# Kernel tuning notes

Hardware: AMD Instinct MI355X
Metric: run time of the kernel (lower is better)

The kernel has to match this reference:

```python
import jax, jax.numpy as jnp
import numpy as np

NUM_HEADS = 8
KEY_DIM = 64
WINDOW = 8
SHIFT = 4
B, H, W, C = 8, 64, 64, 512


def setup_inputs() -> dict:
    key = jax.random.key(0)
    ks = jax.random.split(key, 6)
    s = 0.02  # small init scale for numerically tame attention
    return {
        "x": jax.random.normal(ks[0], (B, H, W, C), jnp.float32),
        "wq": jax.random.normal(ks[1], (C, NUM_HEADS, KEY_DIM), jnp.float32) * s,
        "bq": jnp.zeros((NUM_HEADS, KEY_DIM), jnp.float32),
        "wk": jax.random.normal(ks[2], (C, NUM_HEADS, KEY_DIM), jnp.float32) * s,
        "bk": jnp.zeros((NUM_HEADS, KEY_DIM), jnp.float32),
        "wv": jax.random.normal(ks[3], (C, NUM_HEADS, KEY_DIM), jnp.float32) * s,
        "bv": jnp.zeros((NUM_HEADS, KEY_DIM), jnp.float32),
        "wo": jax.random.normal(ks[4], (NUM_HEADS, KEY_DIM, C), jnp.float32) * s,
        "bo": jnp.zeros((C,), jnp.float32),
    }


def reference(x, wq, bq, wk, bk, wv, bv, wo, bo):
    b, h, w, c = x.shape
    ws, ss = WINDOW, SHIFT
    pad_h = (ws - h % ws) % ws
    pad_w = (ws - w % ws) % ws
    padded = jnp.pad(x, ((0, 0), (0, pad_h), (0, pad_w), (0, 0)))
    if ss:
        padded = jnp.roll(padded, shift=(-ss, -ss), axis=(1, 2))
    ph, pw = h + pad_h, w + pad_w
    nh, nw = ph // ws, pw // ws
    # window partition: [B, nh, ws, nw, ws, C] -> [B*nh*nw, ws*ws, C]
    win = padded.reshape(b, nh, ws, nw, ws, c)
    win = win.transpose(0, 1, 3, 2, 4, 5).reshape(-1, ws * ws, c)
    q = jnp.einsum("ntc,chd->nthd", win, wq) + bq
    k = jnp.einsum("ntc,chd->nthd", win, wk) + bk
    v = jnp.einsum("ntc,chd->nthd", win, wv) + bv
    scale = 1.0 / jnp.sqrt(jnp.asarray(KEY_DIM, q.dtype))
    scores = jnp.einsum("nqhd,nkhd->nhqk", q, k) * scale
    attn = jax.nn.softmax(scores, axis=-1)
    out = jnp.einsum("nhqk,nkhd->nqhd", attn, v)
    proj = jnp.einsum("nqhd,hdc->nqc", out, wo) + bo
    # window merge
    merged = proj.reshape(b, nh, nw, ws, ws, c)
    merged = merged.transpose(0, 1, 3, 2, 4, 5).reshape(b, ph, pw, c)
    if ss:
        merged = jnp.roll(merged, shift=(ss, ss), axis=(1, 2))
    if pad_h or pad_w:
        merged = merged[:, :h, :w, :]
    return x + merged
```

## Files before the change

### kernel.cpp

```cpp
#include <hip/hip_runtime.h>

typedef unsigned short u16;
typedef short bf16x8 __attribute__((ext_vector_type(8)));
typedef float f32x4 __attribute__((ext_vector_type(4)));

typedef __attribute__((address_space(3))) unsigned int lds_uint;
typedef __attribute__((address_space(1))) const unsigned int glob_uint;

__device__ __forceinline__ void gll16(const void* g, void* l) {
    __builtin_amdgcn_global_load_lds((glob_uint*)g, (lds_uint*)l, 16, 0, 0);
}

__device__ __forceinline__ u16 f2b(float f) {
    union { float f; unsigned int u; } cv; cv.f = f;
    unsigned int u = cv.u;
    u += 0x7fffu + ((u >> 16) & 1u);
    return (u16)(u >> 16);
}

__device__ __forceinline__ uint2 pack4(float a, float b, float c, float d) {
    uint2 r;
    r.x = (unsigned int)f2b(a) | ((unsigned int)f2b(b) << 16);
    r.y = (unsigned int)f2b(c) | ((unsigned int)f2b(d) << 16);
    return r;
}

__global__ void prep_kernel(const float* __restrict__ wq, const float* __restrict__ wk,
                            const float* __restrict__ wv, const float* __restrict__ wo,
                            const float* __restrict__ bq, const float* __restrict__ bk,
                            const float* __restrict__ bv,
                            u16* __restrict__ wqkvh, u16* __restrict__ woT,
                            float* __restrict__ biash) {
    int idx = blockIdx.x * 256 + threadIdx.x;
    const int N1 = 512 * 1536;
    const int N2 = 512 * 512;
    if (idx < N1) {
        int k = idx / 1536, n2 = idx % 1536;
        int h = n2 / 192, j = n2 % 192;
        const float* w = (j < 64) ? wq : (j < 128) ? wk : wv;
        wqkvh[(size_t)n2 * 512 + k] = f2b(w[k * 512 + h * 64 + (j & 63)]);
    } else if (idx < N1 + N2) {
        int i = idx - N1;
        int k = i / 512, n = i % 512;
        woT[n * 512 + k] = f2b(wo[k * 512 + n]);
    } else if (idx < N1 + N2 + 1536) {
        int n2 = idx - N1 - N2;
        int h = n2 / 192, j = n2 % 192;
        const float* b = (j < 64) ? bq : (j < 128) ? bk : bv;
        biash[n2] = b[h * 64 + (j & 63)];
    }
}

__global__ __launch_bounds__(256) void pre_kernel(const float* __restrict__ x,
                                                  u16* __restrict__ xw) {
    int idx = blockIdx.x * 256 + threadIdx.x;
    int row = idx >> 6;
    int c = (idx & 63) * 8;
    int b_ = row >> 12, win = (row >> 6) & 63, t = row & 63;
    int wi = win >> 3, wj = win & 7, ti = t >> 3, tj = t & 7;
    int hh = (wi * 8 + ti + 4) & 63, ww = (wj * 8 + tj + 4) & 63;
    const float* src = x + ((size_t)b_ * 4096 + hh * 64 + ww) * 512 + c;
    float4 v0 = *(const float4*)src;
    float4 v1 = *(const float4*)(src + 4);
    ushort4 p0, p1;
    p0.x = f2b(v0.x); p0.y = f2b(v0.y); p0.z = f2b(v0.z); p0.w = f2b(v0.w);
    p1.x = f2b(v1.x); p1.y = f2b(v1.y); p1.z = f2b(v1.z); p1.w = f2b(v1.w);
    u16* dst = xw + (size_t)row * 512 + c;
    *(ushort4*)dst = p0;
    *(ushort4*)(dst + 4) = p1;
}

__global__ __launch_bounds__(256, 4) void fused_qkv_attn(const u16* __restrict__ xw,
        const u16* __restrict__ wqkvh, const float* __restrict__ biash,
        u16* __restrict__ ows) {
    __shared__ u16 S[16384];
    const int tid = threadIdx.x;
    const int lane = tid & 63, wid = tid >> 6;
    const int wr = wid >> 1, wc = wid & 1;
    const int m = lane & 15, qd = lane >> 4;
    const int win = blockIdx.x & 511;
    const int h = blockIdx.x >> 9;
    const int rowBase = win * 64;

    u16* As  = S;
    u16* Bs  = S + 4096;
    u16* QKs = S;
    u16* VT  = S + 8704;
    u16* Pw  = S + wid * 1152;

    const u16* Bsrc = wqkvh + (size_t)h * 192 * 512;
    f32x4 acc[2][6];
#pragma unroll
    for (int i = 0; i < 2; ++i)
#pragma unroll
        for (int j = 0; j < 6; ++j) acc[i][j] = (f32x4){0.f, 0.f, 0.f, 0.f};

    for (int kt = 0; kt < 8; ++kt) {
        const int k0 = kt * 64;
#pragma unroll
        for (int j = 0; j < 2; ++j) {
            int q = j * 256 + tid;
            int r = q >> 3, c = (q & 7) ^ (r & 7);
            gll16(xw + (size_t)(rowBase + r) * 512 + k0 + c * 8, As + q * 8);
        }
#pragma unroll
        for (int j = 0; j < 6; ++j) {
            int q = j * 256 + tid;
            int r = q >> 3, c = (q & 7) ^ (r & 7);
            gll16(Bsrc + (size_t)r * 512 + k0 + c * 8, Bs + q * 8);
        }
        __syncthreads();
#pragma unroll
        for (int s = 0; s < 2; ++s) {
            bf16x8 a[2], b[6];
#pragma unroll
            for (int ni = 0; ni < 6; ++ni) {
                int R = wc * 96 + ni * 16 + m;
                b[ni] = *(const bf16x8*)&Bs[R * 64 + (((s * 4 + qd) ^ (R & 7)) * 8)];
            }
#pragma unroll
            for (int mi = 0; mi < 2; ++mi) {
                int R = wr * 32 + mi * 16 + m;
                a[mi] = *(const bf16x8*)&As[R * 64 + (((s * 4 + qd) ^ (R & 7)) * 8)];
            }
#pragma unroll
            for (int mi = 0; mi < 2; ++mi)
#pragma unroll
                for (int ni = 0; ni < 6; ++ni)
                    acc[mi][ni] = __builtin_amdgcn_mfma_f32_16x16x32_bf16(b[ni], a[mi], acc[mi][ni], 0, 0, 0);
        }
        __syncthreads();
    }

#pragma unroll
    for (int mi = 0; mi < 2; ++mi) {
        int t = wr * 32 + mi * 16 + m;
#pragma unroll
        for (int ni = 0; ni < 6; ++ni) {
            int cn = wc * 96 + ni * 16;
            float4 bb = *(const float4*)&biash[h * 192 + cn + qd * 4];
            if (cn < 128) {
                *(uint2*)&QKs[t * 136 + cn + qd * 4] =
                    pack4(acc[mi][ni][0] + bb.x, acc[mi][ni][1] + bb.y,
                          acc[mi][ni][2] + bb.z, acc[mi][ni][3] + bb.w);
            } else {
                int d0 = cn - 128 + qd * 4;
                VT[(d0 + 0) * 72 + t] = f2b(acc[mi][ni][0] + bb.x);
                VT[(d0 + 1) * 72 + t] = f2b(acc[mi][ni][1] + bb.y);
                VT[(d0 + 2) * 72 + t] = f2b(acc[mi][ni][2] + bb.z);
                VT[(d0 + 3) * 72 + t] = f2b(acc[mi][ni][3] + bb.w);
            }
        }
    }
    __syncthreads();

    const int q0 = wid * 16;
    f32x4 sa[4];
#pragma unroll
    for (int ni = 0; ni < 4; ++ni) sa[ni] = (f32x4){0.f, 0.f, 0.f, 0.f};
#pragma unroll
    for (int s = 0; s < 2; ++s) {
        bf16x8 qf = *(const bf16x8*)&QKs[(q0 + m) * 136 + s * 32 + qd * 8];
#pragma unroll
        for (int ni = 0; ni < 4; ++ni) {
            bf16x8 kf = *(const bf16x8*)&QKs[(ni * 16 + m) * 136 + 64 + s * 32 + qd * 8];
            sa[ni] = __builtin_amdgcn_mfma_f32_16x16x32_bf16(qf, kf, sa[ni], 0, 0, 0);
        }
    }
    __syncthreads();

    const float c1 = 0.125f * 1.4426950408889634f;
#pragma unroll
    for (int rr = 0; rr < 4; ++rr) {
        float mx = -3.4e38f;
#pragma unroll
        for (int ni = 0; ni < 4; ++ni) mx = fmaxf(mx, sa[ni][rr]);
        mx = fmaxf(mx, __shfl_xor(mx, 1, 64));
        mx = fmaxf(mx, __shfl_xor(mx, 2, 64));
        mx = fmaxf(mx, __shfl_xor(mx, 4, 64));
        mx = fmaxf(mx, __shfl_xor(mx, 8, 64));
        float sum = 0.f;
#pragma unroll
        for (int ni = 0; ni < 4; ++ni) {
            float p = exp2f((sa[ni][rr] - mx) * c1);
            sa[ni][rr] = p;
            sum += p;
        }
        sum += __shfl_xor(sum, 1, 64);
        sum += __shfl_xor(sum, 2, 64);
        sum += __shfl_xor(sum, 4, 64);
        sum += __shfl_xor(sum, 8, 64);
        float inv = 1.f / sum;
        int r = qd * 4 + rr;
#pragma unroll
        for (int ni = 0; ni < 4; ++ni)
            Pw[r * 72 + ni * 16 + m] = f2b(sa[ni][rr] * inv);
    }

    f32x4 oa[4];
#pragma unroll
    for (int ni = 0; ni < 4; ++ni) oa[ni] = (f32x4){0.f, 0.f, 0.f, 0.f};
#pragma unroll
    for (int s = 0; s < 2; ++s) {
        bf16x8 pf = *(const bf16x8*)&Pw[m * 72 + s * 32 + qd * 8];
#pragma unroll
        for (int ni = 0; ni < 4; ++ni) {
            bf16x8 vf = *(const bf16x8*)&VT[(ni * 16 + m) * 72 + s * 32 + qd * 8];
            oa[ni] = __builtin_amdgcn_mfma_f32_16x16x32_bf16(vf, pf, oa[ni], 0, 0, 0);
        }
    }
    u16* dst = ows + (size_t)(rowBase + q0 + m) * 512 + h * 64;
#pragma unroll
    for (int ni = 0; ni < 4; ++ni)
        *(uint2*)&dst[ni * 16 + qd * 4] =
            pack4(oa[ni][0], oa[ni][1], oa[ni][2], oa[ni][3]);
}

__global__ __launch_bounds__(256) void proj_gemm(const u16* __restrict__ ows,
        const u16* __restrict__ woT, const float* __restrict__ bo,
        const float* __restrict__ x, float* __restrict__ out) {
    __shared__ u16 S[16384];
    u16* As = S;
    u16* Bs = S + 8192;
    const int tid = threadIdx.x;
    const int lane = tid & 63, wid = tid >> 6;
    const int wr = wid >> 1, wc = wid & 1;
    const int m = lane & 15, qd = lane >> 4;
    const int rowBase = blockIdx.y * 128;
    const int colBase = blockIdx.x * 128;
    const int c8 = (lane & 7) ^ (lane >> 3);

    f32x4 acc[4][4];
#pragma unroll
    for (int i = 0; i < 4; ++i)
#pragma unroll
        for (int j = 0; j < 4; ++j) acc[i][j] = (f32x4){0.f, 0.f, 0.f, 0.f};

    for (int kt = 0; kt < 8; ++kt) {
        const int k0 = kt * 64;
        __syncthreads();
#pragma unroll
        for (int j = 0; j < 4; ++j) {
            int q = (j * 4 + wid) * 64 + lane;
            int r = (j * 4 + wid) * 8 + (lane >> 3);
            gll16(ows + (size_t)(rowBase + r) * 512 + k0 + c8 * 8, &As[q * 8]);
            gll16(woT + (size_t)(colBase + r) * 512 + k0 + c8 * 8, &Bs[q * 8]);
        }
        __syncthreads();
#pragma unroll
        for (int s = 0; s < 2; ++s) {
            bf16x8 a[4], b[4];
#pragma unroll
            for (int ni = 0; ni < 4; ++ni) {
                int R = wc * 64 + ni * 16 + m;
                b[ni] = *(const bf16x8*)&Bs[R * 64 + (((s * 4 + qd) ^ (R & 7)) * 8)];
            }
#pragma unroll
            for (int mi = 0; mi < 4; ++mi) {
                int R = wr * 64 + mi * 16 + m;
                a[mi] = *(const bf16x8*)&As[R * 64 + (((s * 4 + qd) ^ (R & 7)) * 8)];
            }
#pragma unroll
            for (int mi = 0; mi < 4; ++mi)
#pragma unroll
                for (int ni = 0; ni < 4; ++ni)
                    acc[mi][ni] = __builtin_amdgcn_mfma_f32_16x16x32_bf16(b[ni], a[mi], acc[mi][ni], 0, 0, 0);
        }
    }
    __syncthreads();

    float* Ct = (float*)S;
    for (int p = 0; p < 2; ++p) {
        if (wr == p) {
#pragma unroll
            for (int mi = 0; mi < 4; ++mi) {
                int r = mi * 16 + m;
#pragma unroll
                for (int ni = 0; ni < 4; ++ni) {
                    int ch = (wc * 16 + ni * 4 + qd) ^ (r & 7);
                    *(f32x4*)&Ct[r * 128 + ch * 4] = acc[mi][ni];
                }
            }
        }
        __syncthreads();
        {
            int k = tid >> 2, cseg = tid & 3;
            int row = rowBase + p * 64 + k;
            int win = row >> 6, t = row & 63;
            int b_ = win >> 6, wh = (win >> 3) & 7, ww_ = win & 7;
            int ti = t >> 3, tj = t & 7;
            int hh = (wh * 8 + ti + 4) & 63;
            int www = (ww_ * 8 + tj + 4) & 63;
            size_t tok = (size_t)b_ * 4096 + hh * 64 + www;
            const float* xs = &x[tok * 512 + colBase + cseg * 32];
            const float* bs = &bo[colBase + cseg * 32];
            float* os = &out[tok * 512 + colBase + cseg * 32];
#pragma unroll
            for (int j = 0; j < 8; ++j) {
                int ch = (cseg * 8 + j) ^ (k & 7);
                f32x4 c = *(const f32x4*)&Ct[k * 128 + ch * 4];
                float4 xv = *(const float4*)&xs[j * 4];
                float4 bv = *(const float4*)&bs[j * 4];
                float4 o;
                o.x = c[0] + bv.x + xv.x;
                o.y = c[1] + bv.y + xv.y;
                o.z = c[2] + bv.z + xv.z;
                o.w = c[3] + bv.w + xv.w;
                *(float4*)&os[j * 4] = o;
            }
        }
        __syncthreads();
    }
}

extern "C" void kernel_launch(void* const* d_in, const int* in_sizes, int n_in,
                              void* d_out, int out_size, void* d_ws, size_t ws_size,
                              hipStream_t stream) {
    const float* x  = (const float*)d_in[0];
    const float* wq = (const float*)d_in[1];
    const float* bq = (const float*)d_in[2];
    const float* wk = (const float*)d_in[3];
    const float* bk = (const float*)d_in[4];
    const float* wv = (const float*)d_in[5];
    const float* bv = (const float*)d_in[6];
    const float* wo = (const float*)d_in[7];
    const float* bo = (const float*)d_in[8];
    float* out = (float*)d_out;
    char* ws = (char*)d_ws;

    u16*   wqkvh = (u16*)ws;
    u16*   woT   = (u16*)(ws + 1572864);
    float* biash = (float*)(ws + 1572864 + 524288);
    size_t off = 2103296;
    u16* xw  = (u16*)(ws + off);
    u16* ows = xw + (size_t)16777216;

    const int prepN = 512 * 1536 + 512 * 512 + 1536;
    prep_kernel<<<dim3((prepN + 255) / 256), dim3(256), 0, stream>>>(
        wq, wk, wv, wo, bq, bk, bv, wqkvh, woT, biash);
    pre_kernel<<<dim3(8192), dim3(256), 0, stream>>>(x, xw);
    fused_qkv_attn<<<dim3(4096), dim3(256), 0, stream>>>(xw, wqkvh, biash, ows);
    proj_gemm<<<dim3(4, 256), dim3(256), 0, stream>>>(ows, woT, bo, x, out);
}
```

Before: 257.9 us.

## Double-buffer QKV projection K-loop with 32-wide tiles and async prefetch

The QKV GEMM main loop now uses two LDS buffers with 32-wide K tiles. The next tile is prefetched via global_load_lds while the current one is computed, with explicit vmcnt waits and barriers in place of two __syncthreads per iteration. The LDS swizzle changes to match the narrower rows. The aim is to hide global load latency behind MFMA work, at the cost of more loop iterations, more barriers per K, and reliance on hand-tuned waitcnt counts.

```diff
diff --git a/kernel.cpp b/kernel.cpp
--- a/kernel.cpp
+++ b/kernel.cpp
@@ -82,55 +82,84 @@
     const int h = blockIdx.x >> 9;
     const int rowBase = win * 64;
 
-    u16* As  = S;
-    u16* Bs  = S + 4096;
+    u16* const A0 = S;
+    u16* const B0 = S + 2048;
+    u16* const A1 = S + 8192;
+    u16* const B1 = S + 10240;
     u16* QKs = S;
     u16* VT  = S + 8704;
     u16* Pw  = S + wid * 1152;
 
-    const u16* Bsrc = wqkvh + (size_t)h * 192 * 512;
+    const u16* xwRow = xw + (size_t)rowBase * 512;
+    const u16* Bsrc  = wqkvh + (size_t)h * 192 * 512;
+
+    const int rA = tid >> 2;
+    const int cA = (tid & 3) ^ ((rA >> 1) & 3);
+
     f32x4 acc[2][6];
 #pragma unroll
     for (int i = 0; i < 2; ++i)
 #pragma unroll
         for (int j = 0; j < 6; ++j) acc[i][j] = (f32x4){0.f, 0.f, 0.f, 0.f};
 
-    for (int kt = 0; kt < 8; ++kt) {
-        const int k0 = kt * 64;
-#pragma unroll
-        for (int j = 0; j < 2; ++j) {
-            int q = j * 256 + tid;
-            int r = q >> 3, c = (q & 7) ^ (r & 7);
-            gll16(xw + (size_t)(rowBase + r) * 512 + k0 + c * 8, As + q * 8);
-        }
-#pragma unroll
-        for (int j = 0; j < 6; ++j) {
-            int q = j * 256 + tid;
-            int r = q >> 3, c = (q & 7) ^ (r & 7);
-            gll16(Bsrc + (size_t)r * 512 + k0 + c * 8, Bs + q * 8);
-        }
-        __syncthreads();
-#pragma unroll
-        for (int s = 0; s < 2; ++s) {
-            bf16x8 a[2], b[6];
-#pragma unroll
-            for (int ni = 0; ni < 6; ++ni) {
-                int R = wc * 96 + ni * 16 + m;
-                b[ni] = *(const bf16x8*)&Bs[R * 64 + (((s * 4 + qd) ^ (R & 7)) * 8)];
-            }
-#pragma unroll
-            for (int mi = 0; mi < 2; ++mi) {
-                int R = wr * 32 + mi * 16 + m;
-                a[mi] = *(const bf16x8*)&As[R * 64 + (((s * 4 + qd) ^ (R & 7)) * 8)];
-            }
-#pragma unroll
-            for (int mi = 0; mi < 2; ++mi)
-#pragma unroll
-                for (int ni = 0; ni < 6; ++ni)
-                    acc[mi][ni] = __builtin_amdgcn_mfma_f32_16x16x32_bf16(b[ni], a[mi], acc[mi][ni], 0, 0, 0);
-        }
-        __syncthreads();
-    }
+#define STAGE(K0, DA, DB)                                                    \
+    {                                                                        \
+        gll16(xwRow + (size_t)rA * 512 + (K0) + cA * 8, (DA) + tid * 8);     \
+        _Pragma("unroll")                                                    \
+        for (int j = 0; j < 3; ++j) {                                        \
+            int q = j * 256 + tid;                                           \
+            int r = q >> 2;                                                  \
+            int cl = (q & 3) ^ ((r >> 1) & 3);                               \
+            gll16(Bsrc + (size_t)r * 512 + (K0) + cl * 8, (DB) + q * 8);     \
+        }                                                                    \
+    }
+
+#define COMPUTE(SA, SB)                                                      \
+    {                                                                        \
+        bf16x8 a[2], b[6];                                                   \
+        _Pragma("unroll")                                                    \
+        for (int ni = 0; ni < 6; ++ni) {                                     \
+            int R = wc * 96 + ni * 16 + m;                                   \
+            b[ni] = *(const bf16x8*)&(SB)[R * 32 + ((qd ^ ((R >> 1) & 3)) * 8)]; \
+        }                                                                    \
+        _Pragma("unroll")                                                    \
+        for (int mi = 0; mi < 2; ++mi) {                                     \
+            int R = wr * 32 + mi * 16 + m;                                   \
+            a[mi] = *(const bf16x8*)&(SA)[R * 32 + ((qd ^ ((R >> 1) & 3)) * 8)]; \
+        }                                                                    \
+        _Pragma("unroll")                                                    \
+        for (int mi = 0; mi < 2; ++mi)                                       \
+            _Pragma("unroll")                                                \
+            for (int ni = 0; ni < 6; ++ni)                                   \
+                acc[mi][ni] = __builtin_amdgcn_mfma_f32_16x16x32_bf16(       \
+                    b[ni], a[mi], acc[mi][ni], 0, 0, 0);                     \
+    }
+
+    STAGE(0, A0, B0);
+    {
+        u16 *curA = A0, *curB = B0, *nxtA = A1, *nxtB = B1;
+#pragma unroll 1
+        for (int kt = 0; kt < 15; ++kt) {
+            STAGE((kt + 1) * 32, nxtA, nxtB);
+            asm volatile("s_waitcnt vmcnt(4)" ::: "memory");
+            __builtin_amdgcn_s_barrier();
+            __builtin_amdgcn_sched_barrier(0);
+            COMPUTE(curA, curB);
+            asm volatile("s_waitcnt lgkmcnt(0)" ::: "memory");
+            __builtin_amdgcn_sched_barrier(0);
+            __builtin_amdgcn_s_barrier();
+            u16* t;
+            t = curA; curA = nxtA; nxtA = t;
+            t = curB; curB = nxtB; nxtB = t;
+        }
+        asm volatile("s_waitcnt vmcnt(0)" ::: "memory");
+        __builtin_amdgcn_s_barrier();
+        __builtin_amdgcn_sched_barrier(0);
+        COMPUTE(curA, curB);
+    }
+#undef STAGE
+#undef COMPUTE
+    __syncthreads();
 
 #pragma unroll
     for (int mi = 0; mi < 2; ++mi) {
```

New measurement: 266.1 us. 3.2% more time.
